# Performance work log

Measured on AMD Instinct MI355X. Metric: run time of the kernel, lower is better.

## Reference

```python
import jax, jax.numpy as jnp
import numpy as np

D_MODEL = 1024
NHEAD = 16


def unitnorm(v):
    # F.normalize(v, dim=-1): v / max(||v||_2, 1e-12)
    n = jnp.sqrt(jnp.sum(v * v, axis=-1, keepdims=True))
    return v / jnp.maximum(n, 1e-12)


def setup_inputs() -> dict:
    key = jax.random.key(0)
    ks = jax.random.split(key, 14)
    d = D_MODEL
    sc = 1.0 / np.sqrt(d)
    inp = jax.random.normal(ks[0], (2048, 8, d), dtype=jnp.float32)
    def lin(kw, kb, out_dim):
        W = jax.random.uniform(kw, (out_dim, d), minval=-sc, maxval=sc, dtype=jnp.float32)
        b = jax.random.uniform(kb, (out_dim,), minval=-sc, maxval=sc, dtype=jnp.float32)
        return W, b
    Wq_w, Wq_b = lin(ks[1], ks[2], d)
    Wk_w, Wk_b = lin(ks[3], ks[4], d)
    Wv_w, Wv_b = lin(ks[5], ks[6], d)
    Wo_w, Wo_b = lin(ks[7], ks[8], d)
    Ww_w, Ww_b = lin(ks[9], ks[10], NHEAD)
    Wr_w, Wr_b = lin(ks[11], ks[12], NHEAD)
    return {"inp": inp, "Wq_w": Wq_w, "Wq_b": Wq_b, "Wk_w": Wk_w, "Wk_b": Wk_b,
            "Wv_w": Wv_w, "Wv_b": Wv_b, "Wo_w": Wo_w, "Wo_b": Wo_b,
            "Ww_w": Ww_w, "Ww_b": Ww_b, "Wr_w": Wr_w, "Wr_b": Wr_b}


def reference(inp, Wq_w, Wq_b, Wk_w, Wk_b, Wv_w, Wv_b, Wo_w, Wo_b, Ww_w, Ww_b, Wr_w, Wr_b):
    src = inp  # src=None path
    S, B, d = inp.shape
    n = NHEAD
    # torch Linear: x @ W.T + b
    k = (src @ Wk_w.T + Wk_b).reshape(S, B, n, -1)
    v = (src @ Wv_w.T + Wv_b).reshape(S, B, n, -1)
    q = (inp @ Wq_w.T + Wq_b).reshape(S, B, n, -1)
    k = unitnorm(k)
    q = unitnorm(q)
    w = jax.nn.sigmoid(src @ Ww_w.T + Ww_b)            # [S,B,n]
    A = jnp.einsum('sbnq,sbnv->bnvq', k, v * w[:, :, :, None])
    r = jax.nn.sigmoid(inp @ Wr_w.T + Wr_b)            # [S,B,n]
    out = jnp.einsum('sbnq,bnvq->sbnv', q, A) * r[:, :, :, None]
    out = out.reshape(S, B, d)
    out = out @ Wo_w.T + Wo_b
    return (out, A)
```

## Files before the change

kernel.cpp:

```cpp
#include <hip/hip_runtime.h>
#include <cstdint>
#include <cstddef>


typedef __bf16 bf16x8 __attribute__((ext_vector_type(8)));
typedef float  f32x4  __attribute__((ext_vector_type(4)));
typedef unsigned short u16x8 __attribute__((ext_vector_type(8)));
typedef unsigned short u16x4 __attribute__((ext_vector_type(4)));

#define ROWS 16384
#define DM   1024

__device__ __forceinline__ unsigned short f2bf(float f) {
  unsigned int u = __builtin_bit_cast(unsigned int, f);
  u += 0x7FFFu + ((u >> 16) & 1u);
  return (unsigned short)(u >> 16);
}
__device__ __forceinline__ float bf2f(unsigned short h) {
  unsigned int u = ((unsigned int)h) << 16;
  return __builtin_bit_cast(float, u);
}
__device__ __forceinline__ float sigm(float x) { return 1.0f / (1.0f + __expf(-x)); }

__device__ __forceinline__ void gload_lds16(const void* g, void* l) {
  __builtin_amdgcn_global_load_lds((__attribute__((address_space(1))) void*)(g),
                                   (__attribute__((address_space(3))) void*)(l),
                                   16, 0, 0);
}

__global__ __launch_bounds__(256) void k_cast_x(const float* __restrict__ X,
                                                unsigned short* __restrict__ Xb) {
  size_t i = ((size_t)blockIdx.x * 256 + threadIdx.x) * 8;
  f32x4 a = *(const f32x4*)(X + i);
  f32x4 b = *(const f32x4*)(X + i + 4);
  u16x8 o;
  o[0] = f2bf(a[0]); o[1] = f2bf(a[1]); o[2] = f2bf(a[2]); o[3] = f2bf(a[3]);
  o[4] = f2bf(b[0]); o[5] = f2bf(b[1]); o[6] = f2bf(b[2]); o[7] = f2bf(b[3]);
  *(u16x8*)(Xb + i) = o;
}

__global__ __launch_bounds__(256) void k_pack_w(
    const float* __restrict__ Wq, const float* __restrict__ Wk, const float* __restrict__ Wv,
    const float* __restrict__ Wo, const float* __restrict__ Ww, const float* __restrict__ Wr,
    const float* __restrict__ bq, const float* __restrict__ bk, const float* __restrict__ bv,
    const float* __restrict__ bw, const float* __restrict__ br,
    unsigned short* __restrict__ Wpack, float* __restrict__ biasP,
    unsigned short* __restrict__ WRw, float* __restrict__ biasWR,
    unsigned short* __restrict__ Wob) {
  int r = blockIdx.x, t = threadIdx.x;
  const float* src; float bias = 0.0f; unsigned short* dst; float* bdst;
  if (r < 1024)      { src = Wq + (size_t)r * DM;          bias = bq[r];        dst = Wpack + (size_t)r * DM;          bdst = biasP + r; }
  else if (r < 2048) { src = Wk + (size_t)(r - 1024) * DM; bias = bk[r - 1024]; dst = Wpack + (size_t)r * DM;          bdst = biasP + r; }
  else if (r < 3072) { src = Wv + (size_t)(r - 2048) * DM; bias = bv[r - 2048]; dst = Wpack + (size_t)r * DM;          bdst = biasP + r; }
  else if (r < 3088) { src = Ww + (size_t)(r - 3072) * DM; bias = bw[r - 3072]; dst = WRw + (size_t)(r - 3072) * DM;   bdst = biasWR + (r - 3072); }
  else if (r < 3104) { src = Wr + (size_t)(r - 3088) * DM; bias = br[r - 3088]; dst = WRw + (size_t)(r - 3072) * DM;   bdst = biasWR + (r - 3072); }
  else               { src = Wo + (size_t)(r - 3104) * DM;                      dst = Wob + (size_t)(r - 3104) * DM;   bdst = nullptr; }
  int c = t * 4;
  f32x4 v = *(const f32x4*)(src + c);
  u16x4 o;
  o[0] = f2bf(v[0]); o[1] = f2bf(v[1]); o[2] = f2bf(v[2]); o[3] = f2bf(v[3]);
  *(u16x4*)(dst + c) = o;
  if (t == 0 && bdst) *bdst = bias;
}

__global__ __launch_bounds__(256) void k_wr(const unsigned short* __restrict__ Xb,
                                            const unsigned short* __restrict__ WRw,
                                            const float* __restrict__ biasWR,
                                            float* __restrict__ WRf) {
  __shared__ __bf16 sA[128 * 64];
  __shared__ __bf16 sB[32 * 64];
  int t = threadIdx.x, lane = t & 63, wid = t >> 6;
  int m0 = blockIdx.x * 128;
  int l15 = lane & 15, l4 = lane >> 4;
  f32x4 acc[2][2];
#pragma unroll
  for (int i = 0; i < 2; ++i)
#pragma unroll
    for (int j = 0; j < 2; ++j) acc[i][j] = (f32x4){0.f, 0.f, 0.f, 0.f};
  int srow = t >> 3, schunk = (t & 7) * 8;
  for (int kt = 0; kt < DM; kt += 64) {
#pragma unroll
    for (int c = 0; c < 4; ++c)
      gload_lds16(Xb + (size_t)(m0 + c * 32 + srow) * DM + kt + schunk,
                  (void*)(sA + c * 2048 + wid * 512));
    gload_lds16(WRw + (size_t)srow * DM + kt + schunk, (void*)(sB + wid * 512));
    __syncthreads();
#pragma unroll
    for (int ks = 0; ks < 2; ++ks) {
      bf16x8 fa[2], fb[2];
#pragma unroll
      for (int mi = 0; mi < 2; ++mi)
        fa[mi] = *(const bf16x8*)(sA + (wid * 32 + mi * 16 + l15) * 64 + (ks * 4 + l4) * 8);
#pragma unroll
      for (int ni = 0; ni < 2; ++ni)
        fb[ni] = *(const bf16x8*)(sB + (ni * 16 + l15) * 64 + (ks * 4 + l4) * 8);
#pragma unroll
      for (int mi = 0; mi < 2; ++mi)
#pragma unroll
        for (int ni = 0; ni < 2; ++ni)
          acc[mi][ni] = __builtin_amdgcn_mfma_f32_16x16x32_bf16(fa[mi], fb[ni], acc[mi][ni], 0, 0, 0);
    }
    __syncthreads();
  }
#pragma unroll
  for (int mi = 0; mi < 2; ++mi)
#pragma unroll
    for (int e = 0; e < 4; ++e) {
      int row = m0 + wid * 32 + mi * 16 + 4 * l4 + e;
#pragma unroll
      for (int ni = 0; ni < 2; ++ni)
        WRf[(size_t)row * 32 + ni * 16 + l15] = acc[mi][ni][e] + biasWR[ni * 16 + l15];
    }
}


#define VMW(N) asm volatile("s_waitcnt vmcnt(" #N ")" ::: "memory")
#define LGKM0  asm volatile("s_waitcnt lgkmcnt(0)" ::: "memory")
#define SB0    __builtin_amdgcn_sched_barrier(0)

__device__ __forceinline__ void stage3(const unsigned short* __restrict__ Asrc,
                                       const unsigned short* __restrict__ Bsrc,
                                       int kt, __bf16* sm, int rbase, int w) {
#pragma unroll
  for (int c = 0; c < 2; ++c)
    gload_lds16(Asrc + (size_t)c * 128 * DM + kt, (void*)(sm + rbase + c * 4096 + w * 512));
#pragma unroll
  for (int c = 0; c < 2; ++c)
    gload_lds16(Bsrc + (size_t)c * 128 * DM + kt, (void*)(sm + rbase + 8192 + c * 4096 + w * 512));
}

__device__ __forceinline__ void comp3(const __bf16* base, f32x4 (&acc)[8][4],
                                      const int (&aoff)[8], const int (&boff)[4]) {
  bf16x8 fa[8], fb[4];
#pragma unroll
  for (int mi = 0; mi < 8; ++mi) fa[mi] = *(const bf16x8*)(base + aoff[mi]);
#pragma unroll
  for (int ni = 0; ni < 4; ++ni) fb[ni] = *(const bf16x8*)(base + boff[ni]);
  LGKM0; SB0;
  __builtin_amdgcn_s_setprio(1);
#pragma unroll
  for (int mi = 0; mi < 8; ++mi)
#pragma unroll
    for (int ni = 0; ni < 4; ++ni)
      acc[mi][ni] = __builtin_amdgcn_mfma_f32_16x16x32_bf16(fa[mi], fb[ni], acc[mi][ni], 0, 0, 0);
  __builtin_amdgcn_s_setprio(0);
  SB0;
}

__device__ __forceinline__ void gemm_d3(const unsigned short* __restrict__ Ag,
                                        const unsigned short* __restrict__ Bg,
                                        __bf16* sm, f32x4 (&acc)[8][4],
                                        int m0, int n0, int lane, int w) {
  const int wm = w >> 2, wn = w & 3;
  const int l15 = lane & 15, l4 = lane >> 4;
  const int t = w * 64 + lane;
  const int srow = t >> 2;
  const int schunk = ((t & 3) ^ (srow & 3)) * 8;
  const unsigned short* Asrc = Ag + (size_t)(m0 + srow) * DM + schunk;
  const unsigned short* Bsrc = Bg + (size_t)(n0 + srow) * DM + schunk;

  int aoff[8], boff[4];
#pragma unroll
  for (int mi = 0; mi < 8; ++mi) {
    int r = wm * 128 + mi * 16 + l15;
    aoff[mi] = r * 32 + ((l4 ^ (r & 3)) << 3);
  }
#pragma unroll
  for (int ni = 0; ni < 4; ++ni) {
    int r = wn * 64 + ni * 16 + l15;
    boff[ni] = 8192 + r * 32 + ((l4 ^ (r & 3)) << 3);
  }

  stage3(Asrc, Bsrc, 0, sm, 0, w);
  stage3(Asrc, Bsrc, 32, sm, 16384, w);
  VMW(4);
  __builtin_amdgcn_s_barrier();
  SB0;

  int rdb = 0, stb = 32768;
  for (int it = 0; it < 30; ++it) {
    stage3(Asrc, Bsrc, (it + 2) * 32, sm, stb, w);
    comp3(sm + rdb, acc, aoff, boff);
    VMW(4);
    __builtin_amdgcn_s_barrier();
    SB0;
    rdb += 16384; if (rdb == 49152) rdb = 0;
    stb += 16384; if (stb == 49152) stb = 0;
  }
  comp3(sm + rdb, acc, aoff, boff);
  VMW(0);
  __builtin_amdgcn_s_barrier();
  SB0;
  rdb += 16384; if (rdb == 49152) rdb = 0;
  comp3(sm + rdb, acc, aoff, boff);
}

__global__ __launch_bounds__(512, 2) void k_gemm_qkv5(
    const unsigned short* __restrict__ Xb, const unsigned short* __restrict__ Wpack,
    const float* __restrict__ biasP, const float* __restrict__ WRf,
    unsigned short* __restrict__ Qb, unsigned short* __restrict__ Kb,
    unsigned short* __restrict__ Vb) {
  __shared__ __bf16 sm[49152];
  const int t = threadIdx.x, lane = t & 63, w = t >> 6;
  const int wm = w >> 2, wn = w & 3;
  const int l15 = lane & 15, l4 = lane >> 4;
  int orig = blockIdx.x;
  int wg = (orig & 7) * 96 + (orig >> 3);
  const int m0 = (wg & 63) << 8;
  const int n0 = (wg >> 6) << 8;
  f32x4 acc[8][4];
#pragma unroll
  for (int i = 0; i < 8; ++i)
#pragma unroll
    for (int j = 0; j < 4; ++j) acc[i][j] = (f32x4){0.f, 0.f, 0.f, 0.f};
  gemm_d3(Xb, Wpack, sm, acc, m0, n0, lane, w);

  const int colbase = n0 + wn * 64;
  float bb[4];
#pragma unroll
  for (int ni = 0; ni < 4; ++ni) bb[ni] = biasP[colbase + ni * 16 + l15];

  if (colbase < 2048) {
    unsigned short* dstp = (colbase < 1024) ? Qb : Kb;
    int coff = (colbase < 1024) ? colbase : (colbase - 1024);
#pragma unroll
    for (int mi = 0; mi < 8; ++mi)
#pragma unroll
      for (int e = 0; e < 4; ++e) {
        float v[4]; float ssq = 0.f;
#pragma unroll
        for (int ni = 0; ni < 4; ++ni) { v[ni] = acc[mi][ni][e] + bb[ni]; ssq += v[ni] * v[ni]; }
        ssq += __shfl_xor(ssq, 1);
        ssq += __shfl_xor(ssq, 2);
        ssq += __shfl_xor(ssq, 4);
        ssq += __shfl_xor(ssq, 8);
        float sc = 1.0f / fmaxf(sqrtf(ssq), 1e-12f);
        int row = m0 + wm * 128 + mi * 16 + 4 * l4 + e;
#pragma unroll
        for (int ni = 0; ni < 4; ++ni)
          dstp[(size_t)row * DM + coff + ni * 16 + l15] = f2bf(v[ni] * sc);
      }
  } else {
    int hv = (colbase - 2048) >> 6;
    int coff = colbase - 2048;
#pragma unroll
    for (int mi = 0; mi < 8; ++mi)
#pragma unroll
      for (int e = 0; e < 4; ++e) {
        int row = m0 + wm * 128 + mi * 16 + 4 * l4 + e;
        float wgt = sigm(WRf[(size_t)row * 32 + hv]);
#pragma unroll
        for (int ni = 0; ni < 4; ++ni)
          Vb[(size_t)row * DM + coff + ni * 16 + l15] = f2bf((acc[mi][ni][e] + bb[ni]) * wgt);
      }
  }
}

__global__ __launch_bounds__(512, 2) void k_gemm_out5(
    const unsigned short* __restrict__ Ob, const unsigned short* __restrict__ Wob,
    const float* __restrict__ bo, float* __restrict__ Out) {
  __shared__ __bf16 sm[49152];
  const int t = threadIdx.x, lane = t & 63, w = t >> 6;
  const int wm = w >> 2, wn = w & 3;
  const int l15 = lane & 15, l4 = lane >> 4;
  int orig = blockIdx.x;
  int wg = (orig & 7) * 32 + (orig >> 3);
  const int m0 = (wg & 63) << 8;
  const int n0 = (wg >> 6) << 8;
  f32x4 acc[8][4];
#pragma unroll
  for (int i = 0; i < 8; ++i)
#pragma unroll
    for (int j = 0; j < 4; ++j) acc[i][j] = (f32x4){0.f, 0.f, 0.f, 0.f};
  gemm_d3(Ob, Wob, sm, acc, m0, n0, lane, w);

  float bb[4];
#pragma unroll
  for (int ni = 0; ni < 4; ++ni) bb[ni] = bo[n0 + wn * 64 + ni * 16 + l15];
#pragma unroll
  for (int mi = 0; mi < 8; ++mi)
#pragma unroll
    for (int e = 0; e < 4; ++e) {
      int row = m0 + wm * 128 + mi * 16 + 4 * l4 + e;
#pragma unroll
      for (int ni = 0; ni < 4; ++ni) {
        int col = n0 + wn * 64 + ni * 16 + l15;
        Out[(size_t)row * DM + col] = acc[mi][ni][e] + bb[ni];
      }
    }
}

__global__ __launch_bounds__(256, 2) void k_gemm_A(const unsigned short* __restrict__ Kb,
                                                   const unsigned short* __restrict__ Vb,
                                                   float* __restrict__ Apart) {
  __shared__ __bf16 sK[64 * 64];
  __shared__ __bf16 sV[64 * 64];
  int t = threadIdx.x, lane = t & 63, wid = t >> 6;
  int bn = blockIdx.x & 127, sk = blockIdx.x >> 7;
  int b = bn >> 4, n = bn & 15;
  f32x4 acc[4];
#pragma unroll
  for (int j = 0; j < 4; j++) acc[j] = (f32x4){0.f, 0.f, 0.f, 0.f};
  int lrow = lane >> 3, lcol = (lane & 7) * 8;

  for (int st = sk * 1024; st < (sk + 1) * 1024; st += 64) {
#pragma unroll
    for (int c = 0; c < 2; c++) {
      int r0 = wid * 16 + c * 8;
      size_t g = ((size_t)(st + r0 + lrow) * 8 + b) * DM + n * 64 + lcol;
      gload_lds16(Kb + g, (void*)(sK + r0 * 64));
      gload_lds16(Vb + g, (void*)(sV + r0 * 64));
    }
    __syncthreads();
#pragma unroll
    for (int kk = 0; kk < 64; kk += 32) {
      bf16x8 av, bv[4];
#pragma unroll
      for (int e = 0; e < 8; e++)
        av[e] = sV[(kk + 8 * (lane >> 4) + e) * 64 + wid * 16 + (lane & 15)];
#pragma unroll
      for (int jn = 0; jn < 4; jn++)
#pragma unroll
        for (int e = 0; e < 8; e++)
          bv[jn][e] = sK[(kk + 8 * (lane >> 4) + e) * 64 + jn * 16 + (lane & 15)];
#pragma unroll
      for (int jn = 0; jn < 4; jn++)
        acc[jn] = __builtin_amdgcn_mfma_f32_16x16x32_bf16(av, bv[jn], acc[jn], 0, 0, 0);
    }
    __syncthreads();
  }
  float* Ap = Apart + (size_t)(sk * 128 + bn) * 4096;
#pragma unroll
  for (int jn = 0; jn < 4; jn++) {
#pragma unroll
    for (int e = 0; e < 4; e++) {
      int i = wid * 16 + 4 * (lane >> 4) + e;
      int j = jn * 16 + (lane & 15);
      Ap[i * 64 + j] = acc[jn][e];
    }
  }
}

__global__ __launch_bounds__(256) void k_reduceA(const float* __restrict__ Apart,
                                                 float* __restrict__ Aout,
                                                 unsigned short* __restrict__ Abf) {
  int bn = blockIdx.x, t = threadIdx.x;
  size_t base = (size_t)bn * 4096 + t * 16;
#pragma unroll
  for (int j = 0; j < 4; ++j) {
    f32x4 x = *(const f32x4*)(Apart + base + j * 4);
    f32x4 y = *(const f32x4*)(Apart + (size_t)128 * 4096 + base + j * 4);
    x += y;
    *(f32x4*)(Aout + base + j * 4) = x;
    u16x4 o;
    o[0] = f2bf(x[0]); o[1] = f2bf(x[1]); o[2] = f2bf(x[2]); o[3] = f2bf(x[3]);
    *(u16x4*)(Abf + base + j * 4) = o;
  }
}

__global__ __launch_bounds__(256, 2) void k_gemm_o2(const unsigned short* __restrict__ Qb,
                                                    const unsigned short* __restrict__ Abf,
                                                    const float* __restrict__ WRf,
                                                    unsigned short* __restrict__ Ob) {
  __shared__ __bf16 sQ[128 * 64];
  __shared__ __bf16 sA[64 * 64];
  int t = threadIdx.x, lane = t & 63, wid = t >> 6;
  int bn = blockIdx.x & 127, stile = blockIdx.x >> 7;
  int b = bn >> 4, n = bn & 15;
  int s0 = stile * 128;
  int lrow = lane >> 3, lcol = (lane & 7) * 8;
#pragma unroll
  for (int c = 0; c < 4; c++) {
    int r0 = wid * 32 + c * 8;
    gload_lds16(Qb + ((size_t)(s0 + r0 + lrow) * 8 + b) * DM + n * 64 + lcol,
                (void*)(sQ + r0 * 64));
  }
#pragma unroll
  for (int c = 0; c < 2; c++) {
    int r0 = wid * 16 + c * 8;
    gload_lds16(Abf + (size_t)bn * 4096 + (size_t)(r0 + lrow) * 64 + lcol,
                (void*)(sA + r0 * 64));
  }
  __syncthreads();
  f32x4 acc[2][4];
#pragma unroll
  for (int i = 0; i < 2; i++)
#pragma unroll
    for (int j = 0; j < 4; j++) acc[i][j] = (f32x4){0.f, 0.f, 0.f, 0.f};
#pragma unroll
  for (int kk = 0; kk < 64; kk += 32) {
    bf16x8 aq[2], bA[4];
#pragma unroll
    for (int mi = 0; mi < 2; mi++)
      aq[mi] = *(const bf16x8*)(sQ + (wid * 32 + mi * 16 + (lane & 15)) * 64 + kk + 8 * (lane >> 4));
#pragma unroll
    for (int ni = 0; ni < 4; ni++)
      bA[ni] = *(const bf16x8*)(sA + (ni * 16 + (lane & 15)) * 64 + kk + 8 * (lane >> 4));
#pragma unroll
    for (int mi = 0; mi < 2; mi++)
#pragma unroll
      for (int ni = 0; ni < 4; ni++)
        acc[mi][ni] = __builtin_amdgcn_mfma_f32_16x16x32_bf16(aq[mi], bA[ni], acc[mi][ni], 0, 0, 0);
  }
#pragma unroll
  for (int mi = 0; mi < 2; mi++) {
#pragma unroll
    for (int e = 0; e < 4; e++) {
      int srow = wid * 32 + mi * 16 + 4 * (lane >> 4) + e;
      size_t row = (size_t)(s0 + srow) * 8 + b;
      float rv = sigm(WRf[row * 32 + 16 + n]);
#pragma unroll
      for (int ni = 0; ni < 4; ni++)
        Ob[row * DM + n * 64 + ni * 16 + (lane & 15)] = f2bf(acc[mi][ni][e] * rv);
    }
  }
}

extern "C" void kernel_launch(void* const* d_in, const int* in_sizes, int n_in,
                              void* d_out, int out_size, void* d_ws, size_t ws_size,
                              hipStream_t stream) {
  (void)in_sizes; (void)n_in; (void)out_size; (void)ws_size;
  const float* X  = (const float*)d_in[0];
  const float* Wq = (const float*)d_in[1];  const float* bq = (const float*)d_in[2];
  const float* Wk = (const float*)d_in[3];  const float* bk = (const float*)d_in[4];
  const float* Wv = (const float*)d_in[5];  const float* bv = (const float*)d_in[6];
  const float* Wo = (const float*)d_in[7];  const float* bo = (const float*)d_in[8];
  const float* Ww = (const float*)d_in[9];  const float* bw = (const float*)d_in[10];
  const float* Wr = (const float*)d_in[11]; const float* br = (const float*)d_in[12];

  char* ws = (char*)d_ws;
  unsigned short* Wpack = (unsigned short*)(ws + 0);
  float*          Apart = (float*)(ws + 0);
  unsigned short* Abf   = (unsigned short*)(ws + 4194304);
  float*          biasP = (float*)(ws + 6291456);
  unsigned short* WRw   = (unsigned short*)(ws + 6303744);
  float*          biasWR= (float*)(ws + 6369280);
  unsigned short* Wob   = (unsigned short*)(ws + 6369408);
  unsigned short* Xb    = (unsigned short*)(ws + 8466560);
  unsigned short* Ob    = Xb;
  unsigned short* Qb    = (unsigned short*)(ws + 42020992);
  unsigned short* Kb    = (unsigned short*)(ws + 75575424);
  unsigned short* Vb    = (unsigned short*)(ws + 109129856);
  float*          WRf   = (float*)(ws + 142684288);

  float* Out0 = (float*)d_out;
  float* Aout = Out0 + (size_t)ROWS * DM;

  k_cast_x<<<dim3(8192), dim3(256), 0, stream>>>(X, Xb);
  k_pack_w<<<dim3(4128), dim3(256), 0, stream>>>(Wq, Wk, Wv, Wo, Ww, Wr,
                                                 bq, bk, bv, bw, br,
                                                 Wpack, biasP, WRw, biasWR, Wob);
  k_wr<<<dim3(128), dim3(256), 0, stream>>>(Xb, WRw, biasWR, WRf);
  k_gemm_qkv5<<<dim3(768), dim3(512), 0, stream>>>(Xb, Wpack, biasP, WRf, Qb, Kb, Vb);
  k_gemm_A<<<dim3(256), dim3(256), 0, stream>>>(Kb, Vb, Apart);
  k_reduceA<<<dim3(128), dim3(256), 0, stream>>>(Apart, Aout, Abf);
  k_gemm_o2<<<dim3(2048), dim3(256), 0, stream>>>(Qb, Abf, WRf, Ob);
  k_gemm_out5<<<dim3(256), dim3(512), 0, stream>>>(Ob, Wob, bo, Out0);
}
```

Baseline: 246.8 us.

## Deepen GEMM LDS ring to four stages and double-buffer B fragments

The shared GEMM main loop for the QKV and output projections changes from a three-buffer LDS ring to a four-buffer ring, growing shared memory per block from 96KB to 128KB. B fragments are now double-buffered in registers, so the next tile's LDS reads are issued before the current tile's MFMA block, with partial lgkmcnt waits in place of full drains. The LDS XOR swizzle now keys on (row>>1)&3 instead of row&3, which is meant to reduce bank conflicts on fragment reads. The aim is to hide LDS and global latency behind MFMA work, at the cost of more registers, more LDS, and a harder-to-verify prologue and epilogue schedule.

```diff
diff --git a/kernel.cpp b/kernel.cpp
--- a/kernel.cpp
+++ b/kernel.cpp
@@ -114,40 +114,42 @@
 }
 
 
-#define VMW(N) asm volatile("s_waitcnt vmcnt(" #N ")" ::: "memory")
-#define LGKM0  asm volatile("s_waitcnt lgkmcnt(0)" ::: "memory")
-#define SB0    __builtin_amdgcn_sched_barrier(0)
-
-__device__ __forceinline__ void stage3(const unsigned short* __restrict__ Asrc,
+#define VMW(N)  asm volatile("s_waitcnt vmcnt(" #N ")" ::: "memory")
+#define LGKM(N) asm volatile("s_waitcnt lgkmcnt(" #N ")" ::: "memory")
+#define SB0     __builtin_amdgcn_sched_barrier(0)
+
+__device__ __forceinline__ void stageT(const unsigned short* __restrict__ Asrc,
                                        const unsigned short* __restrict__ Bsrc,
-                                       int kt, __bf16* sm, int rbase, int w) {
+                                       int kt, __bf16* sm, int sb, int w) {
 #pragma unroll
   for (int c = 0; c < 2; ++c)
-    gload_lds16(Asrc + (size_t)c * 128 * DM + kt, (void*)(sm + rbase + c * 4096 + w * 512));
+    gload_lds16(Asrc + (size_t)c * 128 * DM + kt, (void*)(sm + sb + c * 4096 + w * 512));
 #pragma unroll
   for (int c = 0; c < 2; ++c)
-    gload_lds16(Bsrc + (size_t)c * 128 * DM + kt, (void*)(sm + rbase + 8192 + c * 4096 + w * 512));
-}
-
-__device__ __forceinline__ void comp3(const __bf16* base, f32x4 (&acc)[8][4],
-                                      const int (&aoff)[8], const int (&boff)[4]) {
-  bf16x8 fa[8], fb[4];
+    gload_lds16(Bsrc + (size_t)c * 128 * DM + kt, (void*)(sm + sb + 8192 + c * 4096 + w * 512));
+}
+
+__device__ __forceinline__ void rdFA(bf16x8 (&fa)[8], const __bf16* base, const int (&aoff)[8]) {
 #pragma unroll
   for (int mi = 0; mi < 8; ++mi) fa[mi] = *(const bf16x8*)(base + aoff[mi]);
+}
+__device__ __forceinline__ void rdFB(bf16x8 (&fb)[4], const __bf16* base, const int (&boff)[4]) {
 #pragma unroll
   for (int ni = 0; ni < 4; ++ni) fb[ni] = *(const bf16x8*)(base + boff[ni]);
-  LGKM0; SB0;
-  __builtin_amdgcn_s_setprio(1);
-#pragma unroll
-  for (int mi = 0; mi < 8; ++mi)
-#pragma unroll
-    for (int ni = 0; ni < 4; ++ni)
-      acc[mi][ni] = __builtin_amdgcn_mfma_f32_16x16x32_bf16(fa[mi], fb[ni], acc[mi][ni], 0, 0, 0);
-  __builtin_amdgcn_s_setprio(0);
-  SB0;
-}
-
-__device__ __forceinline__ void gemm_d3(const unsigned short* __restrict__ Ag,
+}
+
+#define MFMA32(FB)                                                                   \
+  do {                                                                               \
+    __builtin_amdgcn_s_setprio(1);                                                   \
+    _Pragma("unroll") for (int mi = 0; mi < 8; ++mi)                                 \
+    _Pragma("unroll") for (int ni = 0; ni < 4; ++ni)                                 \
+      acc[mi][ni] = __builtin_amdgcn_mfma_f32_16x16x32_bf16(fa[mi], FB[ni],          \
+                                                            acc[mi][ni], 0, 0, 0);  \
+    __builtin_amdgcn_s_setprio(0);                                                   \
+    SB0;                                                                             \
+  } while (0)
+
+__device__ __forceinline__ void gemm_d4(const unsigned short* __restrict__ Ag,
                                         const unsigned short* __restrict__ Bg,
                                         __bf16* sm, f32x4 (&acc)[8][4],
                                         int m0, int n0, int lane, int w) {
@@ -155,7 +157,7 @@
   const int l15 = lane & 15, l4 = lane >> 4;
   const int t = w * 64 + lane;
   const int srow = t >> 2;
-  const int schunk = ((t & 3) ^ (srow & 3)) * 8;
+  const int schunk = ((t & 3) ^ ((srow >> 1) & 3)) * 8;
   const unsigned short* Asrc = Ag + (size_t)(m0 + srow) * DM + schunk;
   const unsigned short* Bsrc = Bg + (size_t)(n0 + srow) * DM + schunk;
 
@@ -163,44 +165,70 @@
 #pragma unroll
   for (int mi = 0; mi < 8; ++mi) {
     int r = wm * 128 + mi * 16 + l15;
-    aoff[mi] = r * 32 + ((l4 ^ (r & 3)) << 3);
+    aoff[mi] = r * 32 + ((l4 ^ ((r >> 1) & 3)) << 3);
   }
 #pragma unroll
   for (int ni = 0; ni < 4; ++ni) {
     int r = wn * 64 + ni * 16 + l15;
-    boff[ni] = 8192 + r * 32 + ((l4 ^ (r & 3)) << 3);
-  }
-
-  stage3(Asrc, Bsrc, 0, sm, 0, w);
-  stage3(Asrc, Bsrc, 32, sm, 16384, w);
+    boff[ni] = 8192 + r * 32 + ((l4 ^ ((r >> 1) & 3)) << 3);
+  }
+
+  bf16x8 fa[8], fbA[4], fbB[4];
+  stageT(Asrc, Bsrc, 0,  sm, 0,     w);
+  stageT(Asrc, Bsrc, 32, sm, 16384, w);
+  stageT(Asrc, Bsrc, 64, sm, 32768, w);
+  VMW(8);
+  __builtin_amdgcn_s_barrier(); SB0;
+  rdFB(fbA, sm, boff);
+  rdFA(fa, sm, aoff);
   VMW(4);
-  __builtin_amdgcn_s_barrier();
-  SB0;
-
-  int rdb = 0, stb = 32768;
-  for (int it = 0; it < 30; ++it) {
-    stage3(Asrc, Bsrc, (it + 2) * 32, sm, stb, w);
-    comp3(sm + rdb, acc, aoff, boff);
+  __builtin_amdgcn_s_barrier(); SB0;
+
+  int sb = 49152;
+  int rb = 16384;
+  for (int i = 0; i < 14; ++i) {
+    stageT(Asrc, Bsrc, (2 * i + 3) * 32, sm, sb, w); sb = (sb + 16384) & 65535;
+    rdFB(fbB, sm + rb, boff);
+    LGKM(4); SB0;
+    MFMA32(fbA);
+    rdFA(fa, sm + rb, aoff); rb = (rb + 16384) & 65535;
     VMW(4);
-    __builtin_amdgcn_s_barrier();
-    SB0;
-    rdb += 16384; if (rdb == 49152) rdb = 0;
-    stb += 16384; if (stb == 49152) stb = 0;
-  }
-  comp3(sm + rdb, acc, aoff, boff);
+    __builtin_amdgcn_s_barrier(); SB0;
+    stageT(Asrc, Bsrc, (2 * i + 4) * 32, sm, sb, w); sb = (sb + 16384) & 65535;
+    rdFB(fbA, sm + rb, boff);
+    LGKM(4); SB0;
+    MFMA32(fbB);
+    rdFA(fa, sm + rb, aoff); rb = (rb + 16384) & 65535;
+    VMW(4);
+    __builtin_amdgcn_s_barrier(); SB0;
+  }
+  stageT(Asrc, Bsrc, 992, sm, sb, w);
+  rdFB(fbB, sm + rb, boff);
+  LGKM(4); SB0;
+  MFMA32(fbA);
+  rdFA(fa, sm + rb, aoff); rb = (rb + 16384) & 65535;
+  VMW(4);
+  __builtin_amdgcn_s_barrier(); SB0;
+  rdFB(fbA, sm + rb, boff);
+  LGKM(4); SB0;
+  MFMA32(fbB);
+  rdFA(fa, sm + rb, aoff); rb = (rb + 16384) & 65535;
   VMW(0);
-  __builtin_amdgcn_s_barrier();
-  SB0;
-  rdb += 16384; if (rdb == 49152) rdb = 0;
-  comp3(sm + rdb, acc, aoff, boff);
-}
-
-__global__ __launch_bounds__(512, 2) void k_gemm_qkv5(
+  __builtin_amdgcn_s_barrier(); SB0;
+  rdFB(fbB, sm + rb, boff);
+  LGKM(4); SB0;
+  MFMA32(fbA);
+  rdFA(fa, sm + rb, aoff);
+  LGKM(0); SB0;
+  MFMA32(fbB);
+}
+
+__global__ __launch_bounds__(512, 2) void k_gemm_qkv6(
     const unsigned short* __restrict__ Xb, const unsigned short* __restrict__ Wpack,
     const float* __restrict__ biasP, const float* __restrict__ WRf,
     unsigned short* __restrict__ Qb, unsigned short* __restrict__ Kb,
     unsigned short* __restrict__ Vb) {
-  __shared__ __bf16 sm[49152];
+  __shared__ __bf16 sm[65536];
   const int t = threadIdx.x, lane = t & 63, w = t >> 6;
   const int wm = w >> 2, wn = w & 3;
   const int l15 = lane & 15, l4 = lane >> 4;
@@ -213,7 +241,7 @@
   for (int i = 0; i < 8; ++i)
 #pragma unroll
     for (int j = 0; j < 4; ++j) acc[i][j] = (f32x4){0.f, 0.f, 0.f, 0.f};
-  gemm_d3(Xb, Wpack, sm, acc, m0, n0, lane, w);
+  gemm_d4(Xb, Wpack, sm, acc, m0, n0, lane, w);
 
   const int colbase = n0 + wn * 64;
   float bb[4];
@@ -256,10 +284,10 @@
   }
 }
 
-__global__ __launch_bounds__(512, 2) void k_gemm_out5(
+__global__ __launch_bounds__(512, 2) void k_gemm_out6(
     const unsigned short* __restrict__ Ob, const unsigned short* __restrict__ Wob,
     const float* __restrict__ bo, float* __restrict__ Out) {
-  __shared__ __bf16 sm[49152];
+  __shared__ __bf16 sm[65536];
   const int t = threadIdx.x, lane = t & 63, w = t >> 6;
   const int wm = w >> 2, wn = w & 3;
   const int l15 = lane & 15, l4 = lane >> 4;
@@ -272,7 +300,7 @@
   for (int i = 0; i < 8; ++i)
 #pragma unroll
     for (int j = 0; j < 4; ++j) acc[i][j] = (f32x4){0.f, 0.f, 0.f, 0.f};
-  gemm_d3(Ob, Wob, sm, acc, m0, n0, lane, w);
+  gemm_d4(Ob, Wob, sm, acc, m0, n0, lane, w);
 
   float bb[4];
 #pragma unroll
@@ -451,9 +479,9 @@
                                                  bq, bk, bv, bw, br,
                                                  Wpack, biasP, WRw, biasWR, Wob);
   k_wr<<<dim3(128), dim3(256), 0, stream>>>(Xb, WRw, biasWR, WRf);
-  k_gemm_qkv5<<<dim3(768), dim3(512), 0, stream>>>(Xb, Wpack, biasP, WRf, Qb, Kb, Vb);
+  k_gemm_qkv6<<<dim3(768), dim3(512), 0, stream>>>(Xb, Wpack, biasP, WRf, Qb, Kb, Vb);
   k_gemm_A<<<dim3(256), dim3(256), 0, stream>>>(Kb, Vb, Apart);
   k_reduceA<<<dim3(128), dim3(256), 0, stream>>>(Apart, Aout, Abf);
   k_gemm_o2<<<dim3(2048), dim3(256), 0, stream>>>(Qb, Abf, WRf, Ob);
-  k_gemm_out5<<<dim3(256), dim3(512), 0, stream>>>(Ob, Wob, bo, Out0);
-}
+  k_gemm_out6<<<dim3(256), dim3(512), 0, stream>>>(Ob, Wob, bo, Out0);
+}
```

New measurement: 241.9 us. -2.0%, faster.

## Fuse X bf16 cast into k_wr and switch GEMMs to 128x128 double-buffered tiles

Applied to the files above, without the earlier changes.

Removes the separate cast kernel by having k_wr convert the fp32 input to bf16, writing it to both global memory and shared memory. The QKV and output projection GEMMs drop the 256x256 triple-buffered 512-thread tile in favour of a simpler 128x128 double-buffered 256-thread tile with more blocks and higher occupancy. The cast now runs on only 128 blocks, which may limit bandwidth. The smaller tiles lose data reuse and the hand-tuned pipelining.

```diff
diff --git a/kernel.cpp b/kernel.cpp
--- a/kernel.cpp
+++ b/kernel.cpp
@@ -26,17 +26,6 @@
   __builtin_amdgcn_global_load_lds((__attribute__((address_space(1))) void*)(g),
                                    (__attribute__((address_space(3))) void*)(l),
                                    16, 0, 0);
-}
-
-__global__ __launch_bounds__(256) void k_cast_x(const float* __restrict__ X,
-                                                unsigned short* __restrict__ Xb) {
-  size_t i = ((size_t)blockIdx.x * 256 + threadIdx.x) * 8;
-  f32x4 a = *(const f32x4*)(X + i);
-  f32x4 b = *(const f32x4*)(X + i + 4);
-  u16x8 o;
-  o[0] = f2bf(a[0]); o[1] = f2bf(a[1]); o[2] = f2bf(a[2]); o[3] = f2bf(a[3]);
-  o[4] = f2bf(b[0]); o[5] = f2bf(b[1]); o[6] = f2bf(b[2]); o[7] = f2bf(b[3]);
-  *(u16x8*)(Xb + i) = o;
 }
 
 __global__ __launch_bounds__(256) void k_pack_w(
@@ -63,9 +52,10 @@
   if (t == 0 && bdst) *bdst = bias;
 }
 
-__global__ __launch_bounds__(256) void k_wr(const unsigned short* __restrict__ Xb,
+__global__ __launch_bounds__(256) void k_wr(const float* __restrict__ X,
                                             const unsigned short* __restrict__ WRw,
                                             const float* __restrict__ biasWR,
+                                            unsigned short* __restrict__ Xb,
                                             float* __restrict__ WRf) {
   __shared__ __bf16 sA[128 * 64];
   __shared__ __bf16 sB[32 * 64];
@@ -78,12 +68,24 @@
 #pragma unroll
     for (int j = 0; j < 2; ++j) acc[i][j] = (f32x4){0.f, 0.f, 0.f, 0.f};
   int srow = t >> 3, schunk = (t & 7) * 8;
+  int xr = t >> 1, xc = (t & 1) * 32;
   for (int kt = 0; kt < DM; kt += 64) {
-#pragma unroll
-    for (int c = 0; c < 4; ++c)
-      gload_lds16(Xb + (size_t)(m0 + c * 32 + srow) * DM + kt + schunk,
-                  (void*)(sA + c * 2048 + wid * 512));
     gload_lds16(WRw + (size_t)srow * DM + kt + schunk, (void*)(sB + wid * 512));
+    const float* xsrc = X + (size_t)(m0 + xr) * DM + kt + xc;
+    f32x4 xv[8];
+#pragma unroll
+    for (int j = 0; j < 8; ++j) xv[j] = *(const f32x4*)(xsrc + j * 4);
+    u16x8 o[4];
+#pragma unroll
+    for (int j = 0; j < 4; ++j) {
+#pragma unroll
+      for (int e = 0; e < 4; ++e) {
+        o[j][e]     = f2bf(xv[2 * j][e]);
+        o[j][e + 4] = f2bf(xv[2 * j + 1][e]);
+      }
+      *(u16x8*)(Xb + (size_t)(m0 + xr) * DM + kt + xc + j * 8) = o[j];
+      *(u16x8*)((unsigned short*)(sA + xr * 64 + xc) + j * 8) = o[j];
+    }
     __syncthreads();
 #pragma unroll
     for (int ks = 0; ks < 2; ++ks) {
@@ -114,108 +116,81 @@
 }
 
 
-#define VMW(N) asm volatile("s_waitcnt vmcnt(" #N ")" ::: "memory")
-#define LGKM0  asm volatile("s_waitcnt lgkmcnt(0)" ::: "memory")
-#define SB0    __builtin_amdgcn_sched_barrier(0)
-
-__device__ __forceinline__ void stage3(const unsigned short* __restrict__ Asrc,
-                                       const unsigned short* __restrict__ Bsrc,
-                                       int kt, __bf16* sm, int rbase, int w) {
-#pragma unroll
-  for (int c = 0; c < 2; ++c)
-    gload_lds16(Asrc + (size_t)c * 128 * DM + kt, (void*)(sm + rbase + c * 4096 + w * 512));
-#pragma unroll
-  for (int c = 0; c < 2; ++c)
-    gload_lds16(Bsrc + (size_t)c * 128 * DM + kt, (void*)(sm + rbase + 8192 + c * 4096 + w * 512));
-}
-
-__device__ __forceinline__ void comp3(const __bf16* base, f32x4 (&acc)[8][4],
-                                      const int (&aoff)[8], const int (&boff)[4]) {
-  bf16x8 fa[8], fb[4];
-#pragma unroll
-  for (int mi = 0; mi < 8; ++mi) fa[mi] = *(const bf16x8*)(base + aoff[mi]);
-#pragma unroll
-  for (int ni = 0; ni < 4; ++ni) fb[ni] = *(const bf16x8*)(base + boff[ni]);
-  LGKM0; SB0;
-  __builtin_amdgcn_s_setprio(1);
-#pragma unroll
-  for (int mi = 0; mi < 8; ++mi)
-#pragma unroll
-    for (int ni = 0; ni < 4; ++ni)
-      acc[mi][ni] = __builtin_amdgcn_mfma_f32_16x16x32_bf16(fa[mi], fb[ni], acc[mi][ni], 0, 0, 0);
-  __builtin_amdgcn_s_setprio(0);
-  SB0;
-}
-
-__device__ __forceinline__ void gemm_d3(const unsigned short* __restrict__ Ag,
+#define STAGE128(P, kt)                                                             \
+  do {                                                                              \
+    _Pragma("unroll") for (int c = 0; c < 2; ++c)                                   \
+      gload_lds16(Asrc + (size_t)(c * 64) * DM + (kt),                              \
+                  (void*)(sm + (P) * 8192 + c * 2048 + w * 512));                   \
+    _Pragma("unroll") for (int c = 0; c < 2; ++c)                                   \
+      gload_lds16(Bsrc + (size_t)(c * 64) * DM + (kt),                              \
+                  (void*)(sm + (P) * 8192 + 4096 + c * 2048 + w * 512));            \
+  } while (0)
+
+__device__ __forceinline__ void gemm128(const unsigned short* __restrict__ Ag,
                                         const unsigned short* __restrict__ Bg,
-                                        __bf16* sm, f32x4 (&acc)[8][4],
+                                        __bf16* sm, f32x4 (&acc)[4][4],
                                         int m0, int n0, int lane, int w) {
-  const int wm = w >> 2, wn = w & 3;
+  const int wr = w >> 1, wc = w & 1;
   const int l15 = lane & 15, l4 = lane >> 4;
   const int t = w * 64 + lane;
   const int srow = t >> 2;
-  const int schunk = ((t & 3) ^ (srow & 3)) * 8;
-  const unsigned short* Asrc = Ag + (size_t)(m0 + srow) * DM + schunk;
-  const unsigned short* Bsrc = Bg + (size_t)(n0 + srow) * DM + schunk;
-
-  int aoff[8], boff[4];
-#pragma unroll
-  for (int mi = 0; mi < 8; ++mi) {
-    int r = wm * 128 + mi * 16 + l15;
-    aoff[mi] = r * 32 + ((l4 ^ (r & 3)) << 3);
+  const int sc = ((t & 3) ^ ((srow >> 1) & 3)) * 8;
+  const unsigned short* Asrc = Ag + (size_t)(m0 + srow) * DM + sc;
+  const unsigned short* Bsrc = Bg + (size_t)(n0 + srow) * DM + sc;
+
+  int aoff[4], boff[4];
+#pragma unroll
+  for (int mi = 0; mi < 4; ++mi) {
+    int r = wr * 64 + mi * 16 + l15;
+    aoff[mi] = r * 32 + ((l4 ^ ((r >> 1) & 3)) << 3);
   }
 #pragma unroll
   for (int ni = 0; ni < 4; ++ni) {
-    int r = wn * 64 + ni * 16 + l15;
-    boff[ni] = 8192 + r * 32 + ((l4 ^ (r & 3)) << 3);
-  }
-
-  stage3(Asrc, Bsrc, 0, sm, 0, w);
-  stage3(Asrc, Bsrc, 32, sm, 16384, w);
-  VMW(4);
-  __builtin_amdgcn_s_barrier();
-  SB0;
-
-  int rdb = 0, stb = 32768;
-  for (int it = 0; it < 30; ++it) {
-    stage3(Asrc, Bsrc, (it + 2) * 32, sm, stb, w);
-    comp3(sm + rdb, acc, aoff, boff);
-    VMW(4);
-    __builtin_amdgcn_s_barrier();
-    SB0;
-    rdb += 16384; if (rdb == 49152) rdb = 0;
-    stb += 16384; if (stb == 49152) stb = 0;
-  }
-  comp3(sm + rdb, acc, aoff, boff);
-  VMW(0);
-  __builtin_amdgcn_s_barrier();
-  SB0;
-  rdb += 16384; if (rdb == 49152) rdb = 0;
-  comp3(sm + rdb, acc, aoff, boff);
-}
-
-__global__ __launch_bounds__(512, 2) void k_gemm_qkv5(
+    int r = wc * 64 + ni * 16 + l15;
+    boff[ni] = 4096 + r * 32 + ((l4 ^ ((r >> 1) & 3)) << 3);
+  }
+
+  STAGE128(0, 0);
+  __syncthreads();
+  for (int kt = 0; kt < 32; ++kt) {
+    int P = kt & 1;
+    if (kt < 31) STAGE128(P ^ 1, (kt + 1) * 32);
+    const __bf16* base = sm + P * 8192;
+    bf16x8 fa[4], fb[4];
+#pragma unroll
+    for (int mi = 0; mi < 4; ++mi) fa[mi] = *(const bf16x8*)(base + aoff[mi]);
+#pragma unroll
+    for (int ni = 0; ni < 4; ++ni) fb[ni] = *(const bf16x8*)(base + boff[ni]);
+#pragma unroll
+    for (int mi = 0; mi < 4; ++mi)
+#pragma unroll
+      for (int ni = 0; ni < 4; ++ni)
+        acc[mi][ni] = __builtin_amdgcn_mfma_f32_16x16x32_bf16(fa[mi], fb[ni], acc[mi][ni], 0, 0, 0);
+    __syncthreads();
+  }
+}
+
+__global__ __launch_bounds__(256, 3) void k_gemm_qkv8(
     const unsigned short* __restrict__ Xb, const unsigned short* __restrict__ Wpack,
     const float* __restrict__ biasP, const float* __restrict__ WRf,
     unsigned short* __restrict__ Qb, unsigned short* __restrict__ Kb,
     unsigned short* __restrict__ Vb) {
-  __shared__ __bf16 sm[49152];
+  __shared__ __bf16 sm[16384];
   const int t = threadIdx.x, lane = t & 63, w = t >> 6;
-  const int wm = w >> 2, wn = w & 3;
+  const int wr = w >> 1, wc = w & 1;
   const int l15 = lane & 15, l4 = lane >> 4;
   int orig = blockIdx.x;
-  int wg = (orig & 7) * 96 + (orig >> 3);
-  const int m0 = (wg & 63) << 8;
-  const int n0 = (wg >> 6) << 8;
-  f32x4 acc[8][4];
-#pragma unroll
-  for (int i = 0; i < 8; ++i)
+  int wg = (orig & 7) * 384 + (orig >> 3);
+  const int m0 = (wg / 24) << 7;
+  const int n0 = (wg % 24) << 7;
+  f32x4 acc[4][4];
+#pragma unroll
+  for (int i = 0; i < 4; ++i)
 #pragma unroll
     for (int j = 0; j < 4; ++j) acc[i][j] = (f32x4){0.f, 0.f, 0.f, 0.f};
-  gemm_d3(Xb, Wpack, sm, acc, m0, n0, lane, w);
-
-  const int colbase = n0 + wn * 64;
+  gemm128(Xb, Wpack, sm, acc, m0, n0, lane, w);
+
+  const int colbase = n0 + wc * 64;
   float bb[4];
 #pragma unroll
   for (int ni = 0; ni < 4; ++ni) bb[ni] = biasP[colbase + ni * 16 + l15];
@@ -224,7 +199,7 @@
     unsigned short* dstp = (colbase < 1024) ? Qb : Kb;
     int coff = (colbase < 1024) ? colbase : (colbase - 1024);
 #pragma unroll
-    for (int mi = 0; mi < 8; ++mi)
+    for (int mi = 0; mi < 4; ++mi)
 #pragma unroll
       for (int e = 0; e < 4; ++e) {
         float v[4]; float ssq = 0.f;
@@ -234,20 +209,20 @@
         ssq += __shfl_xor(ssq, 2);
         ssq += __shfl_xor(ssq, 4);
         ssq += __shfl_xor(ssq, 8);
-        float sc = 1.0f / fmaxf(sqrtf(ssq), 1e-12f);
-        int row = m0 + wm * 128 + mi * 16 + 4 * l4 + e;
+        float sc2 = 1.0f / fmaxf(sqrtf(ssq), 1e-12f);
+        int row = m0 + wr * 64 + mi * 16 + 4 * l4 + e;
 #pragma unroll
         for (int ni = 0; ni < 4; ++ni)
-          dstp[(size_t)row * DM + coff + ni * 16 + l15] = f2bf(v[ni] * sc);
+          dstp[(size_t)row * DM + coff + ni * 16 + l15] = f2bf(v[ni] * sc2);
       }
   } else {
     int hv = (colbase - 2048) >> 6;
     int coff = colbase - 2048;
 #pragma unroll
-    for (int mi = 0; mi < 8; ++mi)
+    for (int mi = 0; mi < 4; ++mi)
 #pragma unroll
       for (int e = 0; e < 4; ++e) {
-        int row = m0 + wm * 128 + mi * 16 + 4 * l4 + e;
+        int row = m0 + wr * 64 + mi * 16 + 4 * l4 + e;
         float wgt = sigm(WRf[(size_t)row * 32 + hv]);
 #pragma unroll
         for (int ni = 0; ni < 4; ++ni)
@@ -256,35 +231,35 @@
   }
 }
 
-__global__ __launch_bounds__(512, 2) void k_gemm_out5(
+__global__ __launch_bounds__(256, 3) void k_gemm_out8(
     const unsigned short* __restrict__ Ob, const unsigned short* __restrict__ Wob,
     const float* __restrict__ bo, float* __restrict__ Out) {
-  __shared__ __bf16 sm[49152];
+  __shared__ __bf16 sm[16384];
   const int t = threadIdx.x, lane = t & 63, w = t >> 6;
-  const int wm = w >> 2, wn = w & 3;
+  const int wr = w >> 1, wc = w & 1;
   const int l15 = lane & 15, l4 = lane >> 4;
   int orig = blockIdx.x;
-  int wg = (orig & 7) * 32 + (orig >> 3);
-  const int m0 = (wg & 63) << 8;
-  const int n0 = (wg >> 6) << 8;
-  f32x4 acc[8][4];
-#pragma unroll
-  for (int i = 0; i < 8; ++i)
+  int wg = (orig & 7) * 128 + (orig >> 3);
+  const int m0 = (wg >> 3) << 7;
+  const int n0 = (wg & 7) << 7;
+  f32x4 acc[4][4];
+#pragma unroll
+  for (int i = 0; i < 4; ++i)
 #pragma unroll
     for (int j = 0; j < 4; ++j) acc[i][j] = (f32x4){0.f, 0.f, 0.f, 0.f};
-  gemm_d3(Ob, Wob, sm, acc, m0, n0, lane, w);
+  gemm128(Ob, Wob, sm, acc, m0, n0, lane, w);
 
   float bb[4];
 #pragma unroll
-  for (int ni = 0; ni < 4; ++ni) bb[ni] = bo[n0 + wn * 64 + ni * 16 + l15];
-#pragma unroll
-  for (int mi = 0; mi < 8; ++mi)
+  for (int ni = 0; ni < 4; ++ni) bb[ni] = bo[n0 + wc * 64 + ni * 16 + l15];
+#pragma unroll
+  for (int mi = 0; mi < 4; ++mi)
 #pragma unroll
     for (int e = 0; e < 4; ++e) {
-      int row = m0 + wm * 128 + mi * 16 + 4 * l4 + e;
+      int row = m0 + wr * 64 + mi * 16 + 4 * l4 + e;
 #pragma unroll
       for (int ni = 0; ni < 4; ++ni) {
-        int col = n0 + wn * 64 + ni * 16 + l15;
+        int col = n0 + wc * 64 + ni * 16 + l15;
         Out[(size_t)row * DM + col] = acc[mi][ni][e] + bb[ni];
       }
     }
@@ -446,14 +421,13 @@
   float* Out0 = (float*)d_out;
   float* Aout = Out0 + (size_t)ROWS * DM;
 
-  k_cast_x<<<dim3(8192), dim3(256), 0, stream>>>(X, Xb);
   k_pack_w<<<dim3(4128), dim3(256), 0, stream>>>(Wq, Wk, Wv, Wo, Ww, Wr,
                                                  bq, bk, bv, bw, br,
                                                  Wpack, biasP, WRw, biasWR, Wob);
-  k_wr<<<dim3(128), dim3(256), 0, stream>>>(Xb, WRw, biasWR, WRf);
-  k_gemm_qkv5<<<dim3(768), dim3(512), 0, stream>>>(Xb, Wpack, biasP, WRf, Qb, Kb, Vb);
+  k_wr<<<dim3(128), dim3(256), 0, stream>>>(X, WRw, biasWR, Xb, WRf);
+  k_gemm_qkv8<<<dim3(3072), dim3(256), 0, stream>>>(Xb, Wpack, biasP, WRf, Qb, Kb, Vb);
   k_gemm_A<<<dim3(256), dim3(256), 0, stream>>>(Kb, Vb, Apart);
   k_reduceA<<<dim3(128), dim3(256), 0, stream>>>(Apart, Aout, Abf);
   k_gemm_o2<<<dim3(2048), dim3(256), 0, stream>>>(Qb, Abf, WRf, Ob);
-  k_gemm_out5<<<dim3(256), dim3(512), 0, stream>>>(Ob, Wob, bo, Out0);
-}
+  k_gemm_out8<<<dim3(1024), dim3(256), 0, stream>>>(Ob, Wob, bo, Out0);
+}
```

Result: slower. 273.3 us (+10.7%).
